# Performance work log

Hardware: AMD Instinct MI355X
Metric: run time of the kernel (lower is better)

## Reference

```python
import jax, jax.numpy as jnp
import numpy as np

B, T, DIM, HID, E = 2, 4096, 1024, 512, 16


def setup_inputs() -> dict:
    key = jax.random.key(0)
    k1, k2, k3, k4 = jax.random.split(key, 4)
    x = jax.random.normal(k1, (B, T, DIM), jnp.float32)
    w1 = jax.random.normal(k2, (E, HID, DIM), jnp.float32) * 0.02
    w2 = jax.random.normal(k3, (E, DIM, HID), jnp.float32) * 0.02
    w3 = jax.random.normal(k4, (E, HID, DIM), jnp.float32) * 0.02
    # Random integer partition of T per batch row: variable-size expert groups
    rng = np.random.default_rng(0)
    cuts = np.sort(rng.integers(0, T, size=(B, E - 1)), axis=1)
    bounds = np.concatenate([np.zeros((B, 1), np.int64), cuts, np.full((B, 1), T, np.int64)], axis=1)
    counts = jnp.asarray(np.diff(bounds, axis=1), jnp.int32)  # [B, E], rows sum to T
    return {"x": x, "num_tokens_per_expert": counts, "w1": w1, "w2": w2, "w3": w3}


def reference(x, num_tokens_per_expert, w1, w2, w3):
    # offsets[b, e] = end of expert e's contiguous token slice in row b
    offsets = jnp.cumsum(num_tokens_per_expert, axis=1).astype(jnp.int32)  # [B, E]
    tok = jnp.arange(x.shape[1])
    # expert owning each token position (tokens are pre-grouped per expert)
    expert_id = jax.vmap(lambda o: jnp.searchsorted(o, tok, side='right'))(offsets)  # [B, T]

    xb = x.astype(jnp.bfloat16)

    def body(acc, scanned):
        e, w1e, w2e, w3e = scanned
        h = jax.nn.silu(xb @ w1e.T) * (xb @ w3e.T)        # [B, T, HID] bf16 SwiGLU
        y = h @ w2e.T                                      # [B, T, DIM]
        acc = acc + jnp.where((expert_id == e)[..., None], y, jnp.bfloat16(0))
        return acc, None

    nE = w1.shape[0]
    acc0 = jnp.zeros(x.shape, jnp.bfloat16)
    out, _ = jax.lax.scan(
        body, acc0,
        (jnp.arange(nE), w1.astype(jnp.bfloat16), w2.astype(jnp.bfloat16), w3.astype(jnp.bfloat16)))
    return out.astype(x.dtype)
```

## Files before the change

### kernel.cpp

```cpp
#include <hip/hip_runtime.h>
#include <hip/hip_bf16.h>
#include <stdint.h>

#define Bq   2
#define Tq   4096
#define DIMq 1024
#define HIDq 512
#define Eq   16
#define Mq   (Bq * Tq)

typedef __attribute__((ext_vector_type(8))) short bf16x8;
typedef __attribute__((ext_vector_type(4))) float f32x4;
typedef unsigned long long ull;

__device__ __forceinline__ unsigned int f2bf(float f) {
  unsigned int u = __builtin_bit_cast(unsigned int, f);
  return (u + 0x7FFFu + ((u >> 16) & 1u)) >> 16;
}
__device__ __forceinline__ float bf2f(unsigned int s) {
  unsigned int u = s << 16;
  return __builtin_bit_cast(float, u);
}
__device__ __forceinline__ ull pack4(const float4 v) {
  return (ull)f2bf(v.x)
       | ((ull)f2bf(v.y) << 16)
       | ((ull)f2bf(v.z) << 32)
       | ((ull)f2bf(v.w) << 48);
}

#define GLOAD16(gp, lp)                                                        \
  __builtin_amdgcn_global_load_lds(                                            \
      (const __attribute__((address_space(1))) unsigned int*)(gp),             \
      (__attribute__((address_space(3))) unsigned int*)(lp), 16, 0, 0)

__global__ __launch_bounds__(256) void convert4_kernel(
    const float* __restrict__ x,  const float* __restrict__ w1,
    const float* __restrict__ w2, const float* __restrict__ w3,
    ull* __restrict__ xb, ull* __restrict__ w1b,
    ull* __restrict__ w2b, ull* __restrict__ w3b) {
  const float* s;
  ull* d;
  switch (blockIdx.y) {
    case 0:  s = x;  d = xb;  break;
    case 1:  s = w1; d = w1b; break;
    case 2:  s = w2; d = w2b; break;
    default: s = w3; d = w3b; break;
  }
  const int N4 = (8388608 / 4);
  for (int i = blockIdx.x * blockDim.x + threadIdx.x; i < N4;
       i += gridDim.x * blockDim.x) {
    float4 v = ((const float4*)s)[i];
    d[i] = pack4(v);
  }
}

__device__ __forceinline__ void chunk_decode(int bid, int& mt, int& nt) {
  const int c = bid & 7;
  const int k = bid >> 3;
  mt = c * 8 + (k >> 3);
  nt = k & 7;
}

__global__ __launch_bounds__(512) void gemm1_kernel(
    const unsigned short* __restrict__ xb, const unsigned short* __restrict__ w1b,
    const unsigned short* __restrict__ w3b, const int* __restrict__ counts,
    unsigned short* __restrict__ hbuf) {
  int mt, nt;
  chunk_decode(blockIdx.x, mt, nt);
  const int t0  = mt * 128;
  const int n0  = nt * 64;
  const int b   = t0 >> 12;
  const int tl0 = t0 & (Tq - 1);

  __shared__ unsigned short As[2][128 * 64];
  __shared__ unsigned short W1s[2][64 * 64];
  __shared__ unsigned short W3s[2][64 * 64];

  const int tid  = threadIdx.x;
  const int lane = tid & 63;
  const int wv   = tid >> 6;
  const int wm2  = (wv >> 1) * 32;
  const int wn2  = (wv & 1) * 32;
  const int q    = lane >> 4;
  const int l15  = lane & 15;
  const int rsw  = (l15 & 7) << 4;

  int lo = 0;
  #pragma unroll 1
  for (int e = 0; e < Eq; ++e) {
    const int hi = lo + counts[b * Eq + e];
    const int s  = lo > tl0 ? lo : tl0;
    const int en = hi < tl0 + 128 ? hi : tl0 + 128;
    lo = hi;
    if (s >= en) continue;

    const unsigned short* __restrict__ w1e = w1b + (size_t)e * HIDq * DIMq;
    const unsigned short* __restrict__ w3e = w3b + (size_t)e * HIDq * DIMq;

    f32x4 acc1[2][2], acc3[2][2];
    #pragma unroll
    for (int i = 0; i < 2; ++i)
      #pragma unroll
      for (int j = 0; j < 2; ++j) { acc1[i][j] = (f32x4)0.f; acc3[i][j] = (f32x4)0.f; }

    auto stage = [&](int k0, int bi) {
      #pragma unroll
      for (int it = 0; it < 2; ++it) {
        const int c = it * 512 + tid;
        const int row = c >> 3;
        const int kc = ((c & 7) << 3) ^ ((row & 7) << 3);
        GLOAD16(xb + (size_t)(t0 + row) * DIMq + k0 + kc,
                (char*)&As[bi][0] + it * 8192 + wv * 1024);
      }
      {
        const int row = tid >> 3;
        const int kc = ((tid & 7) << 3) ^ ((row & 7) << 3);
        GLOAD16(w1e + (size_t)(n0 + row) * DIMq + k0 + kc,
                (char*)&W1s[bi][0] + wv * 1024);
        GLOAD16(w3e + (size_t)(n0 + row) * DIMq + k0 + kc,
                (char*)&W3s[bi][0] + wv * 1024);
      }
    };
    auto compute = [&](int bi) {
      const char* Ab = (const char*)&As[bi][0];
      const char* Ub = (const char*)&W1s[bi][0];
      const char* Vb = (const char*)&W3s[bi][0];
      #pragma unroll
      for (int ks = 0; ks < 2; ++ks) {
        const int kb = (ks * 64 + q * 16) ^ rsw;
        bf16x8 a[2], u[2], v[2];
        #pragma unroll
        for (int i = 0; i < 2; ++i)
          a[i] = *(const bf16x8*)(Ab + (wm2 + i * 16 + l15) * 128 + kb);
        #pragma unroll
        for (int j = 0; j < 2; ++j) {
          u[j] = *(const bf16x8*)(Ub + (wn2 + j * 16 + l15) * 128 + kb);
          v[j] = *(const bf16x8*)(Vb + (wn2 + j * 16 + l15) * 128 + kb);
        }
        #pragma unroll
        for (int i = 0; i < 2; ++i)
          #pragma unroll
          for (int j = 0; j < 2; ++j) {
            acc1[i][j] = __builtin_amdgcn_mfma_f32_16x16x32_bf16(a[i], u[j], acc1[i][j], 0, 0, 0);
            acc3[i][j] = __builtin_amdgcn_mfma_f32_16x16x32_bf16(a[i], v[j], acc3[i][j], 0, 0, 0);
          }
      }
    };

    stage(0, 0);
    __syncthreads();
    int cur = 0;
    #pragma unroll 1
    for (int k0 = 0; k0 < DIMq; k0 += 64) {
      if (k0 + 64 < DIMq) stage(k0 + 64, cur ^ 1);
      compute(cur);
      __syncthreads();
      cur ^= 1;
    }

    const int rlo = s - tl0, rhi = en - tl0;
    #pragma unroll
    for (int i = 0; i < 2; ++i)
      #pragma unroll
      for (int j = 0; j < 2; ++j)
        #pragma unroll
        for (int rr = 0; rr < 4; ++rr) {
          const int row = wm2 + i * 16 + q * 4 + rr;
          if (row >= rlo && row < rhi) {
            const float aa = bf2f(f2bf(acc1[i][j][rr]));
            const float cc = bf2f(f2bf(acc3[i][j][rr]));
            const float sg = bf2f(f2bf(1.f / (1.f + __expf(-aa))));
            const float tt = bf2f(f2bf(aa * sg));
            hbuf[(size_t)(t0 + row) * HIDq + n0 + wn2 + j * 16 + l15] =
                (unsigned short)f2bf(tt * cc);
          }
        }
  }
}

__global__ __launch_bounds__(512) void gemm2_kernel(
    const unsigned short* __restrict__ hb, const unsigned short* __restrict__ w2b,
    const int* __restrict__ counts, float* __restrict__ out) {
  int mt, nt;
  chunk_decode(blockIdx.x, mt, nt);
  const int t0  = mt * 128;
  const int n0  = nt * 128;
  const int b   = t0 >> 12;
  const int tl0 = t0 & (Tq - 1);

  __shared__ unsigned short Hs[2][128 * 64];
  __shared__ unsigned short Bs[2][128 * 64];

  const int tid  = threadIdx.x;
  const int lane = tid & 63;
  const int wv   = tid >> 6;
  const int wm2  = (wv >> 1) * 32;
  const int wn2  = (wv & 1) * 64;
  const int q    = lane >> 4;
  const int l15  = lane & 15;
  const int rsw  = (l15 & 7) << 4;

  int lo = 0;
  #pragma unroll 1
  for (int e = 0; e < Eq; ++e) {
    const int hi = lo + counts[b * Eq + e];
    const int s  = lo > tl0 ? lo : tl0;
    const int en = hi < tl0 + 128 ? hi : tl0 + 128;
    lo = hi;
    if (s >= en) continue;

    const unsigned short* __restrict__ w2e = w2b + (size_t)e * DIMq * HIDq;

    f32x4 acc[2][4];
    #pragma unroll
    for (int i = 0; i < 2; ++i)
      #pragma unroll
      for (int j = 0; j < 4; ++j) acc[i][j] = (f32x4)0.f;

    auto stage = [&](int k0, int bi) {
      #pragma unroll
      for (int it = 0; it < 2; ++it) {
        const int c = it * 512 + tid;
        const int row = c >> 3;
        const int kc = ((c & 7) << 3) ^ ((row & 7) << 3);
        GLOAD16(hb + (size_t)(t0 + row) * HIDq + k0 + kc,
                (char*)&Hs[bi][0] + it * 8192 + wv * 1024);
        GLOAD16(w2e + (size_t)(n0 + row) * HIDq + k0 + kc,
                (char*)&Bs[bi][0] + it * 8192 + wv * 1024);
      }
    };
    auto compute = [&](int bi) {
      const char* Ab = (const char*)&Hs[bi][0];
      const char* Wb = (const char*)&Bs[bi][0];
      #pragma unroll
      for (int ks = 0; ks < 2; ++ks) {
        const int kb = (ks * 64 + q * 16) ^ rsw;
        bf16x8 a[2], w[4];
        #pragma unroll
        for (int i = 0; i < 2; ++i)
          a[i] = *(const bf16x8*)(Ab + (wm2 + i * 16 + l15) * 128 + kb);
        #pragma unroll
        for (int j = 0; j < 4; ++j)
          w[j] = *(const bf16x8*)(Wb + (wn2 + j * 16 + l15) * 128 + kb);
        #pragma unroll
        for (int i = 0; i < 2; ++i)
          #pragma unroll
          for (int j = 0; j < 4; ++j)
            acc[i][j] = __builtin_amdgcn_mfma_f32_16x16x32_bf16(a[i], w[j], acc[i][j], 0, 0, 0);
      }
    };

    stage(0, 0);
    __syncthreads();
    int cur = 0;
    #pragma unroll 1
    for (int k0 = 0; k0 < HIDq; k0 += 64) {
      if (k0 + 64 < HIDq) stage(k0 + 64, cur ^ 1);
      compute(cur);
      __syncthreads();
      cur ^= 1;
    }

    const int rlo = s - tl0, rhi = en - tl0;
    #pragma unroll
    for (int i = 0; i < 2; ++i)
      #pragma unroll
      for (int j = 0; j < 4; ++j)
        #pragma unroll
        for (int rr = 0; rr < 4; ++rr) {
          const int row = wm2 + i * 16 + q * 4 + rr;
          if (row >= rlo && row < rhi) {
            out[(size_t)(t0 + row) * DIMq + n0 + wn2 + j * 16 + l15] =
                bf2f(f2bf(acc[i][j][rr]));
          }
        }
  }
}

extern "C" void kernel_launch(void* const* d_in, const int* in_sizes, int n_in,
                              void* d_out, int out_size, void* d_ws, size_t ws_size,
                              hipStream_t stream) {
  const float* x      = (const float*)d_in[0];
  const int*   counts = (const int*)d_in[1];
  const float* w1     = (const float*)d_in[2];
  const float* w2     = (const float*)d_in[3];
  const float* w3     = (const float*)d_in[4];
  float* out = (float*)d_out;

  char* ws = (char*)d_ws;
  unsigned short* xb  = (unsigned short*)(ws + 256);
  unsigned short* w1b = (unsigned short*)(ws + 256 + (16u << 20));
  unsigned short* w2b = (unsigned short*)(ws + 256 + (32u << 20));
  unsigned short* w3b = (unsigned short*)(ws + 256 + (48u << 20));
  unsigned short* hb  = (unsigned short*)(ws + 256 + (64u << 20));

  convert4_kernel<<<dim3(2048, 4), 256, 0, stream>>>(
      x, w1, w2, w3, (ull*)xb, (ull*)w1b, (ull*)w2b, (ull*)w3b);
  gemm1_kernel<<<512, 512, 0, stream>>>(xb, w1b, w3b, counts, hb);
  gemm2_kernel<<<512, 512, 0, stream>>>(hb, w2b, counts, out);
}
```

Measured before the change: 262.3 us.

## Replace per-tile expert scan with precomputed balanced worklist of (tile, expert) items

A tiny setup kernel enumerates every (token-tile, expert-segment, n-tile) work item and writes them to a global worklist. Both GEMM kernels then split that list evenly across blocks instead of giving each block a fixed tile that loops over all experts it overlaps. The aim is to balance load, since tiles straddling several expert boundaries do several full K loops while others do one. It adds an extra launch and a serial prefix pass. It also changes which blocks share weight and activation data, which may reduce L2 locality.

Result: faster. 231.4 us (-11.8%).

```diff
diff --git a/kernel.cpp b/kernel.cpp
--- a/kernel.cpp
+++ b/kernel.cpp
@@ -54,24 +54,45 @@
   }
 }
 
-__device__ __forceinline__ void chunk_decode(int bid, int& mt, int& nt) {
-  const int c = bid & 7;
-  const int k = bid >> 3;
-  mt = c * 8 + (k >> 3);
-  nt = k & 7;
-}
+__global__ void setup_worklist(const int* __restrict__ counts,
+                               unsigned int* __restrict__ wl) {
+  __shared__ int ns_arr[64];
+  const int t   = threadIdx.x;
+  const int b   = t >> 5;
+  const int tl0 = (t & 31) * 128;
+  int se[16], sl[16], sh[16];
+  int ns = 0, lo = 0;
+  for (int e = 0; e < Eq; ++e) {
+    const int hi = lo + counts[b * Eq + e];
+    const int s  = lo > tl0 ? lo : tl0;
+    const int en = hi < tl0 + 128 ? hi : tl0 + 128;
+    if (s < en) { se[ns] = e; sl[ns] = s - tl0; sh[ns] = en - tl0; ++ns; }
+    lo = hi;
+  }
+  ns_arr[t] = ns;
+  __syncthreads();
+  int off = 0;
+  for (int i = 0; i < t; ++i) off += ns_arr[i];
+  for (int k = 0; k < ns; ++k)
+    for (int nt = 0; nt < 8; ++nt)
+      wl[1 + (off + k) * 8 + nt] =
+          ((unsigned int)t << 24) | ((unsigned int)nt << 21) |
+          ((unsigned int)se[k] << 16) | ((unsigned int)sl[k] << 8) |
+          (unsigned int)sh[k];
+  if (t == 63) wl[0] = (unsigned int)((off + ns) * 8);
+}
+
+#define WORK_LOOP(wlptr)                                                       \
+  const int Nw = (int)wlptr[0];                                                \
+  const int qw = (Nw + 7) >> 3;                                                \
+  const int cx = blockIdx.x & 7, sx = blockIdx.x >> 3;                         \
+  const int jend = min((cx + 1) * qw, Nw);                                     \
+  for (int j = cx * qw + sx; j < jend; j += 64)
 
 __global__ __launch_bounds__(512) void gemm1_kernel(
     const unsigned short* __restrict__ xb, const unsigned short* __restrict__ w1b,
-    const unsigned short* __restrict__ w3b, const int* __restrict__ counts,
+    const unsigned short* __restrict__ w3b, const unsigned int* __restrict__ wl,
     unsigned short* __restrict__ hbuf) {
-  int mt, nt;
-  chunk_decode(blockIdx.x, mt, nt);
-  const int t0  = mt * 128;
-  const int n0  = nt * 64;
-  const int b   = t0 >> 12;
-  const int tl0 = t0 & (Tq - 1);
-
   __shared__ unsigned short As[2][128 * 64];
   __shared__ unsigned short W1s[2][64 * 64];
   __shared__ unsigned short W3s[2][64 * 64];
@@ -85,14 +106,15 @@
   const int l15  = lane & 15;
   const int rsw  = (l15 & 7) << 4;
 
-  int lo = 0;
-  #pragma unroll 1
-  for (int e = 0; e < Eq; ++e) {
-    const int hi = lo + counts[b * Eq + e];
-    const int s  = lo > tl0 ? lo : tl0;
-    const int en = hi < tl0 + 128 ? hi : tl0 + 128;
-    lo = hi;
-    if (s >= en) continue;
+  WORK_LOOP(wl) {
+    const unsigned int it_w = wl[1 + j];
+    const int mt  = it_w >> 24;
+    const int nt  = (it_w >> 21) & 7;
+    const int e   = (it_w >> 16) & 15;
+    const int rlo = (it_w >> 8) & 255;
+    const int rhi = it_w & 255;
+    const int t0  = mt * 128;
+    const int n0  = nt * 64;
 
     const unsigned short* __restrict__ w1e = w1b + (size_t)e * HIDq * DIMq;
     const unsigned short* __restrict__ w3e = w3b + (size_t)e * HIDq * DIMq;
@@ -101,7 +123,7 @@
     #pragma unroll
     for (int i = 0; i < 2; ++i)
       #pragma unroll
-      for (int j = 0; j < 2; ++j) { acc1[i][j] = (f32x4)0.f; acc3[i][j] = (f32x4)0.f; }
+      for (int jj = 0; jj < 2; ++jj) { acc1[i][jj] = (f32x4)0.f; acc3[i][jj] = (f32x4)0.f; }
 
     auto stage = [&](int k0, int bi) {
       #pragma unroll
@@ -133,16 +155,16 @@
         for (int i = 0; i < 2; ++i)
           a[i] = *(const bf16x8*)(Ab + (wm2 + i * 16 + l15) * 128 + kb);
         #pragma unroll
-        for (int j = 0; j < 2; ++j) {
-          u[j] = *(const bf16x8*)(Ub + (wn2 + j * 16 + l15) * 128 + kb);
-          v[j] = *(const bf16x8*)(Vb + (wn2 + j * 16 + l15) * 128 + kb);
+        for (int jj = 0; jj < 2; ++jj) {
+          u[jj] = *(const bf16x8*)(Ub + (wn2 + jj * 16 + l15) * 128 + kb);
+          v[jj] = *(const bf16x8*)(Vb + (wn2 + jj * 16 + l15) * 128 + kb);
         }
         #pragma unroll
         for (int i = 0; i < 2; ++i)
           #pragma unroll
-          for (int j = 0; j < 2; ++j) {
-            acc1[i][j] = __builtin_amdgcn_mfma_f32_16x16x32_bf16(a[i], u[j], acc1[i][j], 0, 0, 0);
-            acc3[i][j] = __builtin_amdgcn_mfma_f32_16x16x32_bf16(a[i], v[j], acc3[i][j], 0, 0, 0);
+          for (int jj = 0; jj < 2; ++jj) {
+            acc1[i][jj] = __builtin_amdgcn_mfma_f32_16x16x32_bf16(a[i], u[jj], acc1[i][jj], 0, 0, 0);
+            acc3[i][jj] = __builtin_amdgcn_mfma_f32_16x16x32_bf16(a[i], v[jj], acc3[i][jj], 0, 0, 0);
           }
       }
     };
@@ -158,20 +180,19 @@
       cur ^= 1;
     }
 
-    const int rlo = s - tl0, rhi = en - tl0;
     #pragma unroll
     for (int i = 0; i < 2; ++i)
       #pragma unroll
-      for (int j = 0; j < 2; ++j)
+      for (int jj = 0; jj < 2; ++jj)
         #pragma unroll
         for (int rr = 0; rr < 4; ++rr) {
           const int row = wm2 + i * 16 + q * 4 + rr;
           if (row >= rlo && row < rhi) {
-            const float aa = bf2f(f2bf(acc1[i][j][rr]));
-            const float cc = bf2f(f2bf(acc3[i][j][rr]));
+            const float aa = bf2f(f2bf(acc1[i][jj][rr]));
+            const float cc = bf2f(f2bf(acc3[i][jj][rr]));
             const float sg = bf2f(f2bf(1.f / (1.f + __expf(-aa))));
             const float tt = bf2f(f2bf(aa * sg));
-            hbuf[(size_t)(t0 + row) * HIDq + n0 + wn2 + j * 16 + l15] =
+            hbuf[(size_t)(t0 + row) * HIDq + n0 + wn2 + jj * 16 + l15] =
                 (unsigned short)f2bf(tt * cc);
           }
         }
@@ -180,14 +201,7 @@
 
 __global__ __launch_bounds__(512) void gemm2_kernel(
     const unsigned short* __restrict__ hb, const unsigned short* __restrict__ w2b,
-    const int* __restrict__ counts, float* __restrict__ out) {
-  int mt, nt;
-  chunk_decode(blockIdx.x, mt, nt);
-  const int t0  = mt * 128;
-  const int n0  = nt * 128;
-  const int b   = t0 >> 12;
-  const int tl0 = t0 & (Tq - 1);
-
+    const unsigned int* __restrict__ wl, float* __restrict__ out) {
   __shared__ unsigned short Hs[2][128 * 64];
   __shared__ unsigned short Bs[2][128 * 64];
 
@@ -200,14 +214,15 @@
   const int l15  = lane & 15;
   const int rsw  = (l15 & 7) << 4;
 
-  int lo = 0;
-  #pragma unroll 1
-  for (int e = 0; e < Eq; ++e) {
-    const int hi = lo + counts[b * Eq + e];
-    const int s  = lo > tl0 ? lo : tl0;
-    const int en = hi < tl0 + 128 ? hi : tl0 + 128;
-    lo = hi;
-    if (s >= en) continue;
+  WORK_LOOP(wl) {
+    const unsigned int it_w = wl[1 + j];
+    const int mt  = it_w >> 24;
+    const int nt  = (it_w >> 21) & 7;
+    const int e   = (it_w >> 16) & 15;
+    const int rlo = (it_w >> 8) & 255;
+    const int rhi = it_w & 255;
+    const int t0  = mt * 128;
+    const int n0  = nt * 128;
 
     const unsigned short* __restrict__ w2e = w2b + (size_t)e * DIMq * HIDq;
 
@@ -215,7 +230,7 @@
     #pragma unroll
     for (int i = 0; i < 2; ++i)
       #pragma unroll
-      for (int j = 0; j < 4; ++j) acc[i][j] = (f32x4)0.f;
+      for (int jj = 0; jj < 4; ++jj) acc[i][jj] = (f32x4)0.f;
 
     auto stage = [&](int k0, int bi) {
       #pragma unroll
@@ -240,13 +255,13 @@
         for (int i = 0; i < 2; ++i)
           a[i] = *(const bf16x8*)(Ab + (wm2 + i * 16 + l15) * 128 + kb);
         #pragma unroll
-        for (int j = 0; j < 4; ++j)
-          w[j] = *(const bf16x8*)(Wb + (wn2 + j * 16 + l15) * 128 + kb);
+        for (int jj = 0; jj < 4; ++jj)
+          w[jj] = *(const bf16x8*)(Wb + (wn2 + jj * 16 + l15) * 128 + kb);
         #pragma unroll
         for (int i = 0; i < 2; ++i)
           #pragma unroll
-          for (int j = 0; j < 4; ++j)
-            acc[i][j] = __builtin_amdgcn_mfma_f32_16x16x32_bf16(a[i], w[j], acc[i][j], 0, 0, 0);
+          for (int jj = 0; jj < 4; ++jj)
+            acc[i][jj] = __builtin_amdgcn_mfma_f32_16x16x32_bf16(a[i], w[jj], acc[i][jj], 0, 0, 0);
       }
     };
 
@@ -261,17 +276,16 @@
       cur ^= 1;
     }
 
-    const int rlo = s - tl0, rhi = en - tl0;
     #pragma unroll
     for (int i = 0; i < 2; ++i)
       #pragma unroll
-      for (int j = 0; j < 4; ++j)
+      for (int jj = 0; jj < 4; ++jj)
         #pragma unroll
         for (int rr = 0; rr < 4; ++rr) {
           const int row = wm2 + i * 16 + q * 4 + rr;
           if (row >= rlo && row < rhi) {
-            out[(size_t)(t0 + row) * DIMq + n0 + wn2 + j * 16 + l15] =
-                bf2f(f2bf(acc[i][j][rr]));
+            out[(size_t)(t0 + row) * DIMq + n0 + wn2 + jj * 16 + l15] =
+                bf2f(f2bf(acc[i][jj][rr]));
           }
         }
   }
@@ -293,9 +307,11 @@
   unsigned short* w2b = (unsigned short*)(ws + 256 + (32u << 20));
   unsigned short* w3b = (unsigned short*)(ws + 256 + (48u << 20));
   unsigned short* hb  = (unsigned short*)(ws + 256 + (64u << 20));
+  unsigned int*   wl  = (unsigned int*)(ws + 256 + (72u << 20));
 
   convert4_kernel<<<dim3(2048, 4), 256, 0, stream>>>(
       x, w1, w2, w3, (ull*)xb, (ull*)w1b, (ull*)w2b, (ull*)w3b);
-  gemm1_kernel<<<512, 512, 0, stream>>>(xb, w1b, w3b, counts, hb);
-  gemm2_kernel<<<512, 512, 0, stream>>>(hb, w2b, counts, out);
-}
+  setup_worklist<<<1, 64, 0, stream>>>(counts, wl);
+  gemm1_kernel<<<512, 512, 0, stream>>>(xb, w1b, w3b, wl, hb);
+  gemm2_kernel<<<512, 512, 0, stream>>>(hb, w2b, wl, out);
+}
```
